# Kernel tuning notes

Measured on AMD Instinct MI355X. Metric: run time of the kernel, lower is better.

Reference implementation:

```python
import jax, jax.numpy as jnp
import numpy as np

D_MODEL = 1024
NUM_HEADS = 16
D_K = D_MODEL // NUM_HEADS


def setup_inputs() -> dict:
    key = jax.random.key(0)
    ks = jax.random.split(key, 12)
    B, S = 2, 2048
    s = 1.0 / np.sqrt(D_MODEL)
    inp = {
        "query": jax.random.normal(ks[0], (B, S, D_MODEL), jnp.float32),
        "key": jax.random.normal(ks[1], (B, S, D_MODEL), jnp.float32),
        "value": jax.random.normal(ks[2], (B, S, D_MODEL), jnp.float32),
        "w_q": jax.random.normal(ks[3], (D_MODEL, D_MODEL), jnp.float32) * s,
        "b_q": jax.random.normal(ks[4], (D_MODEL,), jnp.float32) * 0.01,
        "w_k": jax.random.normal(ks[5], (D_MODEL, D_MODEL), jnp.float32) * s,
        "b_k": jax.random.normal(ks[6], (D_MODEL,), jnp.float32) * 0.01,
        "w_v": jax.random.normal(ks[7], (D_MODEL, D_MODEL), jnp.float32) * s,
        "b_v": jax.random.normal(ks[8], (D_MODEL,), jnp.float32) * 0.01,
        "w_o": jax.random.normal(ks[9], (D_MODEL, D_MODEL), jnp.float32) * s,
        "b_o": jax.random.normal(ks[10], (D_MODEL,), jnp.float32) * 0.01,
    }
    return inp


def _split_heads(x):
    # [B, S, d_model] -> [B, H, S, d_k]
    B, S, _ = x.shape
    return x.reshape(B, S, NUM_HEADS, D_K).transpose(0, 2, 1, 3)


def reference(query, key, value, w_q, b_q, w_k, b_k, w_v, b_v, w_o, b_o):
    B, S, _ = query.shape
    Q = _split_heads(query @ w_q.T + b_q)
    K = _split_heads(key @ w_k.T + b_k)
    V = _split_heads(value @ w_v.T + b_v)
    scale = 1.0 / jnp.sqrt(jnp.asarray(D_K, Q.dtype))
    scores = jnp.einsum("bhqd,bhkd->bhqk", Q, K) * scale  # [B,H,S,S]
    attn = jax.nn.softmax(scores, axis=-1)
    ctx = jnp.einsum("bhqk,bhkd->bhqd", attn, V)
    ctx = ctx.transpose(0, 2, 1, 3).reshape(B, S, D_MODEL)
    return ctx @ w_o.T + b_o
```

## Files before the change

### kernel.cpp

```cpp
#include <hip/hip_runtime.h>
#include <hip/hip_bf16.h>
#include <stdint.h>

#define D_MODEL 1024
#define NHEAD   16
#define DK      64
#define SEQ     2048
#define BATCH   2

using bf16 = __bf16;
typedef __bf16 bf16x8 __attribute__((ext_vector_type(8)));
typedef float  f32x4  __attribute__((ext_vector_type(4)));
typedef float  f32x16 __attribute__((ext_vector_type(16)));
typedef unsigned uintx2 __attribute__((ext_vector_type(2)));

__device__ __forceinline__ unsigned short f2bf(float x) {
  return __builtin_bit_cast(unsigned short, (__bf16)x);
}
__device__ __forceinline__ unsigned pk2bf(float a, float b) {
  return (unsigned)f2bf(a) | ((unsigned)f2bf(b) << 16);
}
__device__ __forceinline__ float uasf(unsigned x) {
  return __builtin_bit_cast(float, x);
}
__device__ __forceinline__ unsigned fasu(float x) {
  return __builtin_bit_cast(unsigned, x);
}

__device__ __forceinline__ void gld_lds16(const void* g, void* l) {
  __builtin_amdgcn_global_load_lds(
      (const __attribute__((address_space(1))) void*)g,
      (__attribute__((address_space(3))) void*)l, 16, 0, 0);
}

__device__ __forceinline__ float xhalf_sum(float x) {
  uintx2 r = __builtin_amdgcn_permlane32_swap(fasu(x), fasu(x), false, false);
  return uasf(r[0]) + uasf(r[1]);
}

#define MHA_PACK(sv, off, dst)                                           \
  {                                                                      \
    float e0 = __builtin_amdgcn_exp2f(sv[off + 0]);                      \
    float e1 = __builtin_amdgcn_exp2f(sv[off + 1]);                      \
    float e2 = __builtin_amdgcn_exp2f(sv[off + 2]);                      \
    float e3 = __builtin_amdgcn_exp2f(sv[off + 3]);                      \
    float e4 = __builtin_amdgcn_exp2f(sv[off + 4]);                      \
    float e5 = __builtin_amdgcn_exp2f(sv[off + 5]);                      \
    float e6 = __builtin_amdgcn_exp2f(sv[off + 6]);                      \
    float e7 = __builtin_amdgcn_exp2f(sv[off + 7]);                      \
    ps += ((e0 + e1) + (e2 + e3)) + ((e4 + e5) + (e6 + e7));             \
    unsigned c0 = pk2bf(e0, e1), c1 = pk2bf(e2, e3);                     \
    unsigned c2 = pk2bf(e4, e5), c3 = pk2bf(e6, e7);                     \
    uintx2 r02 = __builtin_amdgcn_permlane32_swap(c0, c2, false, false); \
    uintx2 r13 = __builtin_amdgcn_permlane32_swap(c1, c3, false, false); \
    uint4 w; w.x = r02[0]; w.y = r13[0]; w.z = r02[1]; w.w = r13[1];     \
    dst = __builtin_bit_cast(bf16x8, w);                                 \
  }

struct ConvArgs {
  const float* src[7];
  bf16* dst[7];
};

__global__ __launch_bounds__(256) void convert_f32_bf16(ConvArgs a) {
  int v = blockIdx.x * 256 + threadIdx.x;
  int seg, off;
  if (v < 3 * 1048576) { seg = v >> 20; off = v & (1048576 - 1); }
  else { int u = v - 3 * 1048576; seg = 3 + (u >> 18); off = u & (262144 - 1); }
  float4 f = ((const float4*)a.src[seg])[off];
  ushort4 o;
  o.x = f2bf(f.x); o.y = f2bf(f.y); o.z = f2bf(f.z); o.w = f2bf(f.w);
  ((ushort4*)a.dst[seg])[off] = o;
}

template <int BM>
__device__ __forceinline__ void gemm_core(
    const bf16* __restrict__ A, const bf16* __restrict__ B,
    const float* __restrict__ bias, void* __restrict__ Cout,
    int mode, int bx, int by, float oscale, char* lds) {
  constexpr int FM   = BM / 32;
  constexpr int ACH  = BM / 32;
  constexpr int HALF = BM * 128 + 16384;
  const int tid  = threadIdx.x;
  const int lane = tid & 63;
  const int wave = tid >> 6;
  const int wr = wave >> 1, wc = wave & 1;
  const int t = lane >> 4, q = lane & 15;

  f32x4 acc[FM][4];
#pragma unroll
  for (int i = 0; i < FM; ++i)
#pragma unroll
    for (int j = 0; j < 4; ++j) acc[i][j] = (f32x4){0.f, 0.f, 0.f, 0.f};

  const char* Abase = (const char*)(A + (size_t)bx * BM * D_MODEL);
  const char* Bbase = (const char*)(B + (size_t)by * 128 * D_MODEL);

  const char* gA[ACH]; char* sA[ACH];
  const char* gB[4];   char* sB[4];
#pragma unroll
  for (int i = 0; i < ACH; ++i) {
    int c = tid + i * 256, row = c >> 3;
    int src = ((c & 7) * 16) ^ ((row & 7) << 4);
    gA[i] = Abase + (size_t)row * (D_MODEL * 2) + src;
    sA[i] = lds + c * 16;
  }
#pragma unroll
  for (int i = 0; i < 4; ++i) {
    int c = tid + i * 256, row = c >> 3;
    int src = ((c & 7) * 16) ^ ((row & 7) << 4);
    gB[i] = Bbase + (size_t)row * (D_MODEL * 2) + src;
    sB[i] = lds + BM * 128 + c * 16;
  }

  const char* aA[FM][2]; const char* aB[4][2];
#pragma unroll
  for (int f = 0; f < FM; ++f)
#pragma unroll
    for (int ks = 0; ks < 2; ++ks) {
      int ra = wr * (BM / 2) + f * 16 + q;
      aA[f][ks] = lds + ra * 128 + ((ks * 64 + t * 16) ^ ((q & 7) << 4));
    }
#pragma unroll
  for (int f = 0; f < 4; ++f)
#pragma unroll
    for (int ks = 0; ks < 2; ++ks) {
      int rb = wc * 64 + f * 16 + q;
      aB[f][ks] = lds + BM * 128 + rb * 128 + ((ks * 64 + t * 16) ^ ((q & 7) << 4));
    }

#pragma unroll
  for (int i = 0; i < ACH; ++i) gld_lds16(gA[i], sA[i]);
#pragma unroll
  for (int i = 0; i < 4; ++i)  gld_lds16(gB[i], sB[i]);
  __syncthreads();

  auto ktile = [&](int kt, int CUR) {
    if (kt + 1 < D_MODEL / 64) {
      int NXT = CUR ^ HALF;
#pragma unroll
      for (int i = 0; i < ACH; ++i) gld_lds16(gA[i] + (kt + 1) * 128, sA[i] + NXT);
#pragma unroll
      for (int i = 0; i < 4; ++i)  gld_lds16(gB[i] + (kt + 1) * 128, sB[i] + NXT);
    }
#pragma unroll
    for (int ks = 0; ks < 2; ++ks) {
      bf16x8 af[FM], bfv[4];
#pragma unroll
      for (int f = 0; f < FM; ++f) af[f] = *(const bf16x8*)(aA[f][ks] + CUR);
#pragma unroll
      for (int f = 0; f < 4; ++f)  bfv[f] = *(const bf16x8*)(aB[f][ks] + CUR);
      __builtin_amdgcn_s_setprio(1);
#pragma unroll
      for (int fm = 0; fm < FM; ++fm)
#pragma unroll
        for (int fn = 0; fn < 4; ++fn)
          acc[fm][fn] = __builtin_amdgcn_mfma_f32_16x16x32_bf16(
              af[fm], bfv[fn], acc[fm][fn], 0, 0, 0);
      __builtin_amdgcn_s_setprio(0);
    }
    __syncthreads();
  };
  for (int kt = 0; kt < D_MODEL / 64; kt += 2) {
    ktile(kt, 0);
    ktile(kt + 1, HALF);
  }

#pragma unroll
  for (int fm = 0; fm < FM; ++fm)
#pragma unroll
    for (int fn = 0; fn < 4; ++fn)
#pragma unroll
      for (int jj = 0; jj < 4; ++jj) {
        int m = bx * BM + wr * (BM / 2) + fm * 16 + t * 4 + jj;
        int n = by * 128 + wc * 64 + fn * 16 + q;
        float v = acc[fm][fn][jj];
        if (mode == 0) {
          v = (v + bias[n]) * oscale;
          int b = m >> 11, s = m & (SEQ - 1), h = n >> 6, d = n & 63;
          ((bf16*)Cout)[(((size_t)(b * NHEAD + h)) * SEQ + s) * DK + d] = (bf16)v;
        } else if (mode == 1) {
          v += bias[m];
          int h = m >> 6, d = m & 63, b = n >> 11, s = n & (SEQ - 1);
          ((bf16*)Cout)[(((size_t)(b * NHEAD + h)) * DK + d) * SEQ + s] = (bf16)v;
        } else {
          v += bias[n];
          ((float*)Cout)[(size_t)m * D_MODEL + n] = v;
        }
      }
}

struct QkvArgs {
  const bf16* A[3]; const bf16* B[3]; const float* bias[3]; bf16* out[3];
};

__global__ __launch_bounds__(256, 2) void gemm_qkv(QkvArgs a) {
  __shared__ char lds[2 * (128 * 128 + 16384)];
  int z = blockIdx.z;
  int mode = (z == 2) ? 1 : 0;
  int bx = (z == 2) ? blockIdx.y : blockIdx.x;
  int by = (z == 2) ? blockIdx.x : blockIdx.y;
  float osc = (z == 0) ? 0.18033688011112042f : 1.0f;
  gemm_core<128>(a.A[z], a.B[z], a.bias[z], a.out[z], mode, bx, by, osc, lds);
}

__global__ __launch_bounds__(256, 2) void gemm_o(
    const bf16* __restrict__ A, const bf16* __restrict__ B,
    const float* __restrict__ bias, float* __restrict__ Cout) {
  __shared__ char lds[2 * (64 * 128 + 16384)];
  gemm_core<64>(A, B, bias, Cout, 2, blockIdx.x, blockIdx.y, 1.0f, lds);
}

__global__ __launch_bounds__(512, 2) void flash_attn(
    const bf16* __restrict__ Qh, const bf16* __restrict__ Kh,
    const bf16* __restrict__ Vt, bf16* __restrict__ ctx) {
  __shared__ char lds[65536];
  const int tid  = threadIdx.x;
  const int lane = tid & 63;
  const int wave = tid >> 6;
  const int lo = lane & 31;
  const int hi = lane >> 5;
  const int grp = wave >> 2;
  const int wq  = wave & 3;
  const int bh = blockIdx.x;
  const int q0 = blockIdx.y * 128 + wq * 32;

  const bf16* Qb = Qh + (size_t)bh * SEQ * DK;
  const char* Kb = (const char*)(Kh + (size_t)bh * SEQ * DK) + grp * 1024 * 128;
  const char* Vb = (const char*)(Vt + (size_t)bh * DK * SEQ) + grp * 1024 * 2;
  char* Kg = lds + grp * 16384;
  char* Vg = lds + 32768 + grp * 16384;

  bf16x8 qf[4];
#pragma unroll
  for (int c = 0; c < 4; ++c)
    qf[c] = *(const bf16x8*)(Qb + (size_t)(q0 + lo) * DK + c * 16 + hi * 8);

  const int tg = tid & 255;
  const int srow = tg >> 3;
  const int ssrc = ((tg & 7) * 16) ^ ((srow & 7) << 4);
  const char* gK0 = Kb + (size_t)srow * 128 + ssrc;
  const char* gK1 = Kb + (size_t)(srow + 32) * 128 + ssrc;
  const char* gV0 = Vb + (size_t)srow * 4096 + ssrc;
  const char* gV1 = Vb + (size_t)(srow + 32) * 4096 + ssrc;
  char* sK0 = Kg + tg * 16;
  char* sK1 = Kg + 4096 + tg * 16;
  char* sV0 = Vg + tg * 16;
  char* sV1 = Vg + 4096 + tg * 16;

  const int key = (lo & 7) << 4;
  const char* KA[4]; const char* VA[4];
#pragma unroll
  for (int c = 0; c < 4; ++c) {
    int o = (((2 * c + hi) * 16) ^ key) + lo * 128;
    KA[c] = Kg + o;
    VA[c] = Vg + o;
  }

  f32x16 acc0 = {}, acc1 = {};
  float lsum = 0.f;

  gld_lds16(gK0, sK0); gld_lds16(gK1, sK1);
  gld_lds16(gV0, sV0); gld_lds16(gV1, sV1);
  __syncthreads();

  auto tile = [&](int kt, int CUR) {
    if (kt + 1 < 16) {
      int nb = CUR ^ 8192;
      gld_lds16(gK0 + (kt + 1) * 8192, sK0 + nb);
      gld_lds16(gK1 + (kt + 1) * 8192, sK1 + nb);
      gld_lds16(gV0 + (kt + 1) * 128,  sV0 + nb);
      gld_lds16(gV1 + (kt + 1) * 128,  sV1 + nb);
    }

    float ps = 0.f;
    bf16x8 pa[4];

    {
      bf16x8 kf[4];
#pragma unroll
      for (int c = 0; c < 4; ++c) kf[c] = *(const bf16x8*)(KA[c] + CUR);
      f32x16 s0 = {};
      __builtin_amdgcn_s_setprio(1);
#pragma unroll
      for (int c = 0; c < 4; ++c)
        s0 = __builtin_amdgcn_mfma_f32_32x32x16_bf16(kf[c], qf[c], s0, 0, 0, 0);
      __builtin_amdgcn_s_setprio(0);
      MHA_PACK(s0, 0, pa[0]);
      MHA_PACK(s0, 8, pa[1]);
    }

    {
      bf16x8 kf[4];
#pragma unroll
      for (int c = 0; c < 4; ++c) kf[c] = *(const bf16x8*)(KA[c] + CUR + 4096);
      f32x16 s1 = {};
      __builtin_amdgcn_s_setprio(1);
#pragma unroll
      for (int c = 0; c < 4; ++c)
        s1 = __builtin_amdgcn_mfma_f32_32x32x16_bf16(kf[c], qf[c], s1, 0, 0, 0);
      __builtin_amdgcn_s_setprio(0);
      MHA_PACK(s1, 0, pa[2]);
      MHA_PACK(s1, 8, pa[3]);
    }
    lsum += ps;

    bf16x8 vf[2][4];
#pragma unroll
    for (int ks = 0; ks < 4; ++ks) {
      vf[0][ks] = *(const bf16x8*)(VA[ks] + CUR);
      vf[1][ks] = *(const bf16x8*)(VA[ks] + CUR + 4096);
    }
    __builtin_amdgcn_s_setprio(1);
#pragma unroll
    for (int ks = 0; ks < 4; ++ks) {
      acc0 = __builtin_amdgcn_mfma_f32_32x32x16_bf16(pa[ks], vf[0][ks], acc0, 0, 0, 0);
      acc1 = __builtin_amdgcn_mfma_f32_32x32x16_bf16(pa[ks], vf[1][ks], acc1, 0, 0, 0);
    }
    __builtin_amdgcn_s_setprio(0);

    __syncthreads();
  };

  for (int kt = 0; kt < 16; kt += 2) {
    tile(kt, 0);
    tile(kt + 1, 8192);
  }

  float lrun = xhalf_sum(lsum);

  float* lsh = (float*)lds;
  float* U1  = (float*)(lds + 4096);
  if (hi == 0) lsh[grp * 128 + wq * 32 + lo] = lrun;
  if (grp == 1) {
    float* dst = U1 + (size_t)(wq * 64 + lane) * 33;
#pragma unroll
    for (int r = 0; r < 16; ++r) { dst[r] = acc0[r]; dst[16 + r] = acc1[r]; }
  }
  __syncthreads();
  if (grp == 0) {
    const float* src = U1 + (size_t)(wq * 64 + lane) * 33;
    int b = bh >> 4, h = bh & 15;
#pragma unroll
    for (int r = 0; r < 16; ++r) {
      int row = (r & 3) + 8 * (r >> 2) + 4 * hi;
      int gr = wq * 32 + row;
      float linv = 1.f / (lsh[gr] + lsh[128 + gr]);
      float o0 = (acc0[r] + src[r]) * linv;
      float o1 = (acc1[r] + src[16 + r]) * linv;
      int srw = q0 + row;
      size_t base = ((size_t)(b * SEQ + srw)) * D_MODEL + h * 64 + lo;
      ctx[base]      = (bf16)o0;
      ctx[base + 32] = (bf16)o1;
    }
  }
}

extern "C" void kernel_launch(void* const* d_in, const int* in_sizes, int n_in,
                              void* d_out, int out_size, void* d_ws, size_t ws_size,
                              hipStream_t stream) {
  const float* query = (const float*)d_in[0];
  const float* key_  = (const float*)d_in[1];
  const float* value = (const float*)d_in[2];
  const float* w_q = (const float*)d_in[3];
  const float* b_q = (const float*)d_in[4];
  const float* w_k = (const float*)d_in[5];
  const float* b_k = (const float*)d_in[6];
  const float* w_v = (const float*)d_in[7];
  const float* b_v = (const float*)d_in[8];
  const float* w_o = (const float*)d_in[9];
  const float* b_o = (const float*)d_in[10];

  char* ws = (char*)d_ws;
  const size_t MB = 1024 * 1024;
  bf16* bQ  = (bf16*)(ws + 0 * MB);
  bf16* bK  = (bf16*)(ws + 8 * MB);
  bf16* bV  = (bf16*)(ws + 16 * MB);
  bf16* bWq = (bf16*)(ws + 24 * MB);
  bf16* bWk = (bf16*)(ws + 26 * MB);
  bf16* bWv = (bf16*)(ws + 28 * MB);
  bf16* bWo = (bf16*)(ws + 30 * MB);
  bf16* Qh  = (bf16*)(ws + 32 * MB);
  bf16* Kh  = (bf16*)(ws + 40 * MB);
  bf16* Vth = (bf16*)(ws + 48 * MB);
  bf16* ctx = (bf16*)(ws + 56 * MB);

  ConvArgs ca;
  ca.src[0] = query; ca.src[1] = key_; ca.src[2] = value;
  ca.src[3] = w_q;   ca.src[4] = w_k;  ca.src[5] = w_v; ca.src[6] = w_o;
  ca.dst[0] = bQ;  ca.dst[1] = bK;  ca.dst[2] = bV;
  ca.dst[3] = bWq; ca.dst[4] = bWk; ca.dst[5] = bWv; ca.dst[6] = bWo;
  convert_f32_bf16<<<16384, 256, 0, stream>>>(ca);

  QkvArgs qa;
  qa.A[0] = bQ;  qa.B[0] = bWq; qa.bias[0] = b_q; qa.out[0] = Qh;
  qa.A[1] = bK;  qa.B[1] = bWk; qa.bias[1] = b_k; qa.out[1] = Kh;
  qa.A[2] = bWv; qa.B[2] = bV;  qa.bias[2] = b_v; qa.out[2] = Vth;
  gemm_qkv<<<dim3(32, 8, 3), 256, 0, stream>>>(qa);

  flash_attn<<<dim3(32, 16), 512, 0, stream>>>(Qh, Kh, Vth, ctx);

  gemm_o<<<dim3(64, 8), 256, 0, stream>>>(ctx, bWo, b_o, (float*)d_out);
}
```

Measured before the change: 136.3 us.

## Fuse f32-to-bf16 conversion into GEMM tile loads, drop convert kernel

Removes the standalone conversion kernel and has the QKV and output-projection GEMMs read f32 inputs and weights directly. They convert to bf16 in registers before storing into the LDS double buffer. This avoids a full extra read/write pass over inputs and weights plus a launch. In exchange it replaces the asynchronous global-to-LDS loads with register-staged loads and doubles the bytes fetched per tile, raising register pressure and latency exposure in the GEMM main loop.

```diff
diff --git a/kernel.cpp b/kernel.cpp
--- a/kernel.cpp
+++ b/kernel.cpp
@@ -25,6 +25,12 @@
 }
 __device__ __forceinline__ unsigned fasu(float x) {
   return __builtin_bit_cast(unsigned, x);
+}
+__device__ __forceinline__ uint4 cvt8(float4 x, float4 y) {
+  uint4 w;
+  w.x = pk2bf(x.x, x.y); w.y = pk2bf(x.z, x.w);
+  w.z = pk2bf(y.x, y.y); w.w = pk2bf(y.z, y.w);
+  return w;
 }
 
 __device__ __forceinline__ void gld_lds16(const void* g, void* l) {
@@ -57,30 +63,15 @@
     dst = __builtin_bit_cast(bf16x8, w);                                 \
   }
 
-struct ConvArgs {
-  const float* src[7];
-  bf16* dst[7];
-};
-
-__global__ __launch_bounds__(256) void convert_f32_bf16(ConvArgs a) {
-  int v = blockIdx.x * 256 + threadIdx.x;
-  int seg, off;
-  if (v < 3 * 1048576) { seg = v >> 20; off = v & (1048576 - 1); }
-  else { int u = v - 3 * 1048576; seg = 3 + (u >> 18); off = u & (262144 - 1); }
-  float4 f = ((const float4*)a.src[seg])[off];
-  ushort4 o;
-  o.x = f2bf(f.x); o.y = f2bf(f.y); o.z = f2bf(f.z); o.w = f2bf(f.w);
-  ((ushort4*)a.dst[seg])[off] = o;
-}
-
-template <int BM>
+template <int BM, bool AF32, bool BF32>
 __device__ __forceinline__ void gemm_core(
-    const bf16* __restrict__ A, const bf16* __restrict__ B,
+    const void* __restrict__ A, const void* __restrict__ B,
     const float* __restrict__ bias, void* __restrict__ Cout,
     int mode, int bx, int by, float oscale, char* lds) {
   constexpr int FM   = BM / 32;
   constexpr int ACH  = BM / 32;
   constexpr int HALF = BM * 128 + 16384;
+  constexpr int NKT  = D_MODEL / 64;
   const int tid  = threadIdx.x;
   const int lane = tid & 63;
   const int wave = tid >> 6;
@@ -93,8 +84,8 @@
 #pragma unroll
     for (int j = 0; j < 4; ++j) acc[i][j] = (f32x4){0.f, 0.f, 0.f, 0.f};
 
-  const char* Abase = (const char*)(A + (size_t)bx * BM * D_MODEL);
-  const char* Bbase = (const char*)(B + (size_t)by * 128 * D_MODEL);
+  const char* Ab = (const char*)A + (size_t)bx * BM * D_MODEL * (AF32 ? 4 : 2);
+  const char* Bb = (const char*)B + (size_t)by * 128 * D_MODEL * (BF32 ? 4 : 2);
 
   const char* gA[ACH]; char* sA[ACH];
   const char* gB[4];   char* sB[4];
@@ -102,14 +93,16 @@
   for (int i = 0; i < ACH; ++i) {
     int c = tid + i * 256, row = c >> 3;
     int src = ((c & 7) * 16) ^ ((row & 7) << 4);
-    gA[i] = Abase + (size_t)row * (D_MODEL * 2) + src;
+    gA[i] = AF32 ? Ab + (size_t)row * 4096 + 2 * src
+                 : Ab + (size_t)row * 2048 + src;
     sA[i] = lds + c * 16;
   }
 #pragma unroll
   for (int i = 0; i < 4; ++i) {
     int c = tid + i * 256, row = c >> 3;
     int src = ((c & 7) * 16) ^ ((row & 7) << 4);
-    gB[i] = Bbase + (size_t)row * (D_MODEL * 2) + src;
+    gB[i] = BF32 ? Bb + (size_t)row * 4096 + 2 * src
+                 : Bb + (size_t)row * 2048 + src;
     sB[i] = lds + BM * 128 + c * 16;
   }
 
@@ -129,19 +122,49 @@
       aB[f][ks] = lds + BM * 128 + rb * 128 + ((ks * 64 + t * 16) ^ ((q & 7) << 4));
     }
 
-#pragma unroll
-  for (int i = 0; i < ACH; ++i) gld_lds16(gA[i], sA[i]);
-#pragma unroll
-  for (int i = 0; i < 4; ++i)  gld_lds16(gB[i], sB[i]);
+  if constexpr (AF32) {
+#pragma unroll
+    for (int i = 0; i < ACH; ++i)
+      *(uint4*)sA[i] = cvt8(*(const float4*)gA[i], *(const float4*)(gA[i] + 16));
+  } else {
+#pragma unroll
+    for (int i = 0; i < ACH; ++i) gld_lds16(gA[i], sA[i]);
+  }
+  if constexpr (BF32) {
+#pragma unroll
+    for (int i = 0; i < 4; ++i)
+      *(uint4*)sB[i] = cvt8(*(const float4*)gB[i], *(const float4*)(gB[i] + 16));
+  } else {
+#pragma unroll
+    for (int i = 0; i < 4; ++i) gld_lds16(gB[i], sB[i]);
+  }
   __syncthreads();
 
   auto ktile = [&](int kt, int CUR) {
-    if (kt + 1 < D_MODEL / 64) {
-      int NXT = CUR ^ HALF;
-#pragma unroll
-      for (int i = 0; i < ACH; ++i) gld_lds16(gA[i] + (kt + 1) * 128, sA[i] + NXT);
-#pragma unroll
-      for (int i = 0; i < 4; ++i)  gld_lds16(gB[i] + (kt + 1) * 128, sB[i] + NXT);
+    const bool more = kt + 1 < NKT;
+    const int NXT = CUR ^ HALF;
+    float4 fa0[ACH], fa1[ACH], fb0[4], fb1[4];
+    if (more) {
+      if constexpr (AF32) {
+#pragma unroll
+        for (int i = 0; i < ACH; ++i) {
+          fa0[i] = *(const float4*)(gA[i] + (kt + 1) * 256);
+          fa1[i] = *(const float4*)(gA[i] + (kt + 1) * 256 + 16);
+        }
+      } else {
+#pragma unroll
+        for (int i = 0; i < ACH; ++i) gld_lds16(gA[i] + (kt + 1) * 128, sA[i] + NXT);
+      }
+      if constexpr (BF32) {
+#pragma unroll
+        for (int i = 0; i < 4; ++i) {
+          fb0[i] = *(const float4*)(gB[i] + (kt + 1) * 256);
+          fb1[i] = *(const float4*)(gB[i] + (kt + 1) * 256 + 16);
+        }
+      } else {
+#pragma unroll
+        for (int i = 0; i < 4; ++i) gld_lds16(gB[i] + (kt + 1) * 128, sB[i] + NXT);
+      }
     }
 #pragma unroll
     for (int ks = 0; ks < 2; ++ks) {
@@ -159,9 +182,19 @@
               af[fm], bfv[fn], acc[fm][fn], 0, 0, 0);
       __builtin_amdgcn_s_setprio(0);
     }
+    if (more) {
+      if constexpr (AF32) {
+#pragma unroll
+        for (int i = 0; i < ACH; ++i) *(uint4*)(sA[i] + NXT) = cvt8(fa0[i], fa1[i]);
+      }
+      if constexpr (BF32) {
+#pragma unroll
+        for (int i = 0; i < 4; ++i) *(uint4*)(sB[i] + NXT) = cvt8(fb0[i], fb1[i]);
+      }
+    }
     __syncthreads();
   };
-  for (int kt = 0; kt < D_MODEL / 64; kt += 2) {
+  for (int kt = 0; kt < NKT; kt += 2) {
     ktile(kt, 0);
     ktile(kt + 1, HALF);
   }
@@ -191,7 +224,7 @@
 }
 
 struct QkvArgs {
-  const bf16* A[3]; const bf16* B[3]; const float* bias[3]; bf16* out[3];
+  const float* A[3]; const float* B[3]; const float* bias[3]; bf16* out[3];
 };
 
 __global__ __launch_bounds__(256, 2) void gemm_qkv(QkvArgs a) {
@@ -201,14 +234,16 @@
   int bx = (z == 2) ? blockIdx.y : blockIdx.x;
   int by = (z == 2) ? blockIdx.x : blockIdx.y;
   float osc = (z == 0) ? 0.18033688011112042f : 1.0f;
-  gemm_core<128>(a.A[z], a.B[z], a.bias[z], a.out[z], mode, bx, by, osc, lds);
+  gemm_core<128, true, true>(a.A[z], a.B[z], a.bias[z], a.out[z],
+                             mode, bx, by, osc, lds);
 }
 
 __global__ __launch_bounds__(256, 2) void gemm_o(
-    const bf16* __restrict__ A, const bf16* __restrict__ B,
+    const bf16* __restrict__ A, const float* __restrict__ B,
     const float* __restrict__ bias, float* __restrict__ Cout) {
   __shared__ char lds[2 * (64 * 128 + 16384)];
-  gemm_core<64>(A, B, bias, Cout, 2, blockIdx.x, blockIdx.y, 1.0f, lds);
+  gemm_core<64, false, true>(A, B, bias, Cout, 2, blockIdx.x, blockIdx.y,
+                             1.0f, lds);
 }
 
 __global__ __launch_bounds__(512, 2) void flash_attn(
@@ -373,32 +408,18 @@
 
   char* ws = (char*)d_ws;
   const size_t MB = 1024 * 1024;
-  bf16* bQ  = (bf16*)(ws + 0 * MB);
-  bf16* bK  = (bf16*)(ws + 8 * MB);
-  bf16* bV  = (bf16*)(ws + 16 * MB);
-  bf16* bWq = (bf16*)(ws + 24 * MB);
-  bf16* bWk = (bf16*)(ws + 26 * MB);
-  bf16* bWv = (bf16*)(ws + 28 * MB);
-  bf16* bWo = (bf16*)(ws + 30 * MB);
-  bf16* Qh  = (bf16*)(ws + 32 * MB);
-  bf16* Kh  = (bf16*)(ws + 40 * MB);
-  bf16* Vth = (bf16*)(ws + 48 * MB);
-  bf16* ctx = (bf16*)(ws + 56 * MB);
-
-  ConvArgs ca;
-  ca.src[0] = query; ca.src[1] = key_; ca.src[2] = value;
-  ca.src[3] = w_q;   ca.src[4] = w_k;  ca.src[5] = w_v; ca.src[6] = w_o;
-  ca.dst[0] = bQ;  ca.dst[1] = bK;  ca.dst[2] = bV;
-  ca.dst[3] = bWq; ca.dst[4] = bWk; ca.dst[5] = bWv; ca.dst[6] = bWo;
-  convert_f32_bf16<<<16384, 256, 0, stream>>>(ca);
+  bf16* Qh  = (bf16*)(ws + 0 * MB);
+  bf16* Kh  = (bf16*)(ws + 8 * MB);
+  bf16* Vth = (bf16*)(ws + 16 * MB);
+  bf16* ctx = (bf16*)(ws + 24 * MB);
 
   QkvArgs qa;
-  qa.A[0] = bQ;  qa.B[0] = bWq; qa.bias[0] = b_q; qa.out[0] = Qh;
-  qa.A[1] = bK;  qa.B[1] = bWk; qa.bias[1] = b_k; qa.out[1] = Kh;
-  qa.A[2] = bWv; qa.B[2] = bV;  qa.bias[2] = b_v; qa.out[2] = Vth;
+  qa.A[0] = query; qa.B[0] = w_q;   qa.bias[0] = b_q; qa.out[0] = Qh;
+  qa.A[1] = key_;  qa.B[1] = w_k;   qa.bias[1] = b_k; qa.out[1] = Kh;
+  qa.A[2] = w_v;   qa.B[2] = value; qa.bias[2] = b_v; qa.out[2] = Vth;
   gemm_qkv<<<dim3(32, 8, 3), 256, 0, stream>>>(qa);
 
   flash_attn<<<dim3(32, 16), 512, 0, stream>>>(Qh, Kh, Vth, ctx);
 
-  gemm_o<<<dim3(64, 8), 256, 0, stream>>>(ctx, bWo, b_o, (float*)d_out);
-}
+  gemm_o<<<dim3(64, 8), 256, 0, stream>>>(ctx, w_o, b_o, (float*)d_out);
+}
```

After: 151.9 us. 1.11x slower.

## Give QKV projection GEMM a dedicated triple-buffered K-32 pipeline with smaller LDS

Applied to the files above, without the earlier changes.

Adds a separate GEMM core for the QKV projections that streams K in 32-wide tiles through a three-stage LDS ring, using asynchronous global-to-LDS loads two tiles ahead with one barrier per tile. This replaces the previous two-tile-per-iteration scheme that used much more LDS. The aim is to overlap memory traffic with MFMA and reduce LDS footprint so more blocks fit per CU. The output GEMM core is simplified to the fp32 mode only. The risk is more barriers per K step and less MFMA work per synchronisation.

```diff
diff --git a/kernel.cpp b/kernel.cpp
--- a/kernel.cpp
+++ b/kernel.cpp
@@ -73,11 +73,125 @@
   ((ushort4*)a.dst[seg])[off] = o;
 }
 
+__device__ __forceinline__ void gemm_qkv_core(
+    const bf16* __restrict__ A, const bf16* __restrict__ B,
+    const float* __restrict__ bias, bf16* __restrict__ Cout,
+    int mode, int bx, int by, float oscale, char* lds) {
+  constexpr int BUF = 16384;
+  constexpr int NKT = D_MODEL / 32;
+  const int tid  = threadIdx.x;
+  const int lane = tid & 63;
+  const int wave = tid >> 6;
+  const int wr = wave >> 1, wc = wave & 1;
+  const int t = lane >> 4, q = lane & 15;
+
+  f32x4 acc[4][4];
+#pragma unroll
+  for (int i = 0; i < 4; ++i)
+#pragma unroll
+    for (int j = 0; j < 4; ++j) acc[i][j] = (f32x4){0.f, 0.f, 0.f, 0.f};
+
+  const char* Abase = (const char*)(A + (size_t)bx * 128 * D_MODEL);
+  const char* Bbase = (const char*)(B + (size_t)by * 128 * D_MODEL);
+
+  const char* gA[2]; char* sA[2]; const char* gB[2]; char* sB[2];
+#pragma unroll
+  for (int i = 0; i < 2; ++i) {
+    int c = tid + i * 256, row = c >> 2;
+    int src = ((c & 3) * 16) ^ ((row & 3) << 4);
+    gA[i] = Abase + (size_t)row * (D_MODEL * 2) + src;
+    sA[i] = lds + c * 16;
+    gB[i] = Bbase + (size_t)row * (D_MODEL * 2) + src;
+    sB[i] = lds + 8192 + c * 16;
+  }
+
+  const char* aA[4]; const char* aB[4];
+#pragma unroll
+  for (int f = 0; f < 4; ++f) {
+    int ra = wr * 64 + f * 16 + q;
+    aA[f] = lds + ra * 64 + ((t * 16) ^ ((q & 3) << 4));
+    int rb = wc * 64 + f * 16 + q;
+    aB[f] = lds + 8192 + rb * 64 + ((t * 16) ^ ((q & 3) << 4));
+  }
+
+#pragma unroll
+  for (int i = 0; i < 2; ++i) { gld_lds16(gA[i], sA[i]); gld_lds16(gB[i], sB[i]); }
+#pragma unroll
+  for (int i = 0; i < 2; ++i) {
+    gld_lds16(gA[i] + 64, sA[i] + BUF); gld_lds16(gB[i] + 64, sB[i] + BUF);
+  }
+  asm volatile("s_waitcnt vmcnt(4)" ::: "memory");
+  __builtin_amdgcn_s_barrier();
+
+#pragma unroll
+  for (int kt = 0; kt < NKT; ++kt) {
+    const int CUR = (kt % 3) * BUF;
+    if (kt + 2 < NKT) {
+      const int NB = ((kt + 2) % 3) * BUF;
+#pragma unroll
+      for (int i = 0; i < 2; ++i) {
+        gld_lds16(gA[i] + (kt + 2) * 64, sA[i] + NB);
+        gld_lds16(gB[i] + (kt + 2) * 64, sB[i] + NB);
+      }
+    }
+    bf16x8 af[4], bfv[4];
+#pragma unroll
+    for (int f = 0; f < 4; ++f) af[f]  = *(const bf16x8*)(aA[f] + CUR);
+#pragma unroll
+    for (int f = 0; f < 4; ++f) bfv[f] = *(const bf16x8*)(aB[f] + CUR);
+    __builtin_amdgcn_s_setprio(1);
+#pragma unroll
+    for (int fm = 0; fm < 4; ++fm)
+#pragma unroll
+      for (int fn = 0; fn < 4; ++fn)
+        acc[fm][fn] = __builtin_amdgcn_mfma_f32_16x16x32_bf16(
+            af[fm], bfv[fn], acc[fm][fn], 0, 0, 0);
+    __builtin_amdgcn_s_setprio(0);
+    if (kt + 2 < NKT)      asm volatile("s_waitcnt vmcnt(4)" ::: "memory");
+    else if (kt + 1 < NKT) asm volatile("s_waitcnt vmcnt(0)" ::: "memory");
+    __builtin_amdgcn_s_barrier();
+  }
+
+#pragma unroll
+  for (int fm = 0; fm < 4; ++fm)
+#pragma unroll
+    for (int fn = 0; fn < 4; ++fn)
+#pragma unroll
+      for (int jj = 0; jj < 4; ++jj) {
+        int m = bx * 128 + wr * 64 + fm * 16 + t * 4 + jj;
+        int n = by * 128 + wc * 64 + fn * 16 + q;
+        float v = acc[fm][fn][jj];
+        if (mode == 0) {
+          v = (v + bias[n]) * oscale;
+          int b = m >> 11, s = m & (SEQ - 1), h = n >> 6, d = n & 63;
+          Cout[(((size_t)(b * NHEAD + h)) * SEQ + s) * DK + d] = (bf16)v;
+        } else {
+          v += bias[m];
+          int h = m >> 6, d = m & 63, b = n >> 11, s = n & (SEQ - 1);
+          Cout[(((size_t)(b * NHEAD + h)) * DK + d) * SEQ + s] = (bf16)v;
+        }
+      }
+}
+
+struct QkvArgs {
+  const bf16* A[3]; const bf16* B[3]; const float* bias[3]; bf16* out[3];
+};
+
+__global__ __launch_bounds__(256, 2) void gemm_qkv(QkvArgs a) {
+  __shared__ char lds[3 * 16384];
+  int z = blockIdx.z;
+  int mode = (z == 2) ? 1 : 0;
+  int bx = (z == 2) ? blockIdx.y : blockIdx.x;
+  int by = (z == 2) ? blockIdx.x : blockIdx.y;
+  float osc = (z == 0) ? 0.18033688011112042f : 1.0f;
+  gemm_qkv_core(a.A[z], a.B[z], a.bias[z], a.out[z], mode, bx, by, osc, lds);
+}
+
 template <int BM>
 __device__ __forceinline__ void gemm_core(
     const bf16* __restrict__ A, const bf16* __restrict__ B,
-    const float* __restrict__ bias, void* __restrict__ Cout,
-    int mode, int bx, int by, float oscale, char* lds) {
+    const float* __restrict__ bias, float* __restrict__ Cout,
+    int bx, int by, char* lds) {
   constexpr int FM   = BM / 32;
   constexpr int ACH  = BM / 32;
   constexpr int HALF = BM * 128 + 16384;
@@ -174,41 +288,15 @@
       for (int jj = 0; jj < 4; ++jj) {
         int m = bx * BM + wr * (BM / 2) + fm * 16 + t * 4 + jj;
         int n = by * 128 + wc * 64 + fn * 16 + q;
-        float v = acc[fm][fn][jj];
-        if (mode == 0) {
-          v = (v + bias[n]) * oscale;
-          int b = m >> 11, s = m & (SEQ - 1), h = n >> 6, d = n & 63;
-          ((bf16*)Cout)[(((size_t)(b * NHEAD + h)) * SEQ + s) * DK + d] = (bf16)v;
-        } else if (mode == 1) {
-          v += bias[m];
-          int h = m >> 6, d = m & 63, b = n >> 11, s = n & (SEQ - 1);
-          ((bf16*)Cout)[(((size_t)(b * NHEAD + h)) * DK + d) * SEQ + s] = (bf16)v;
-        } else {
-          v += bias[n];
-          ((float*)Cout)[(size_t)m * D_MODEL + n] = v;
-        }
+        Cout[(size_t)m * D_MODEL + n] = acc[fm][fn][jj] + bias[n];
       }
-}
-
-struct QkvArgs {
-  const bf16* A[3]; const bf16* B[3]; const float* bias[3]; bf16* out[3];
-};
-
-__global__ __launch_bounds__(256, 2) void gemm_qkv(QkvArgs a) {
-  __shared__ char lds[2 * (128 * 128 + 16384)];
-  int z = blockIdx.z;
-  int mode = (z == 2) ? 1 : 0;
-  int bx = (z == 2) ? blockIdx.y : blockIdx.x;
-  int by = (z == 2) ? blockIdx.x : blockIdx.y;
-  float osc = (z == 0) ? 0.18033688011112042f : 1.0f;
-  gemm_core<128>(a.A[z], a.B[z], a.bias[z], a.out[z], mode, bx, by, osc, lds);
 }
 
 __global__ __launch_bounds__(256, 2) void gemm_o(
     const bf16* __restrict__ A, const bf16* __restrict__ B,
     const float* __restrict__ bias, float* __restrict__ Cout) {
   __shared__ char lds[2 * (64 * 128 + 16384)];
-  gemm_core<64>(A, B, bias, Cout, 2, blockIdx.x, blockIdx.y, 1.0f, lds);
+  gemm_core<64>(A, B, bias, Cout, blockIdx.x, blockIdx.y, lds);
 }
 
 __global__ __launch_bounds__(512, 2) void flash_attn(
```

New measurement: 125.9 us. 7.6% less time.
